# Kernel optimization log

Measured on AMD Instinct MI355X. Metric: run time of the kernel, lower is better.

## Reference

```python
import jax, jax.numpy as jnp
import numpy as np

W = 4           # cp_size (simulated ranks)
NUM_HEADS = 32
HEAD_SIZE = 128
NUM_KV_HEADS = 8
BLOCK_SIZE = 16
NUM_BLOCKS = 1024
MAX_BLOCKS = 32
MAX_CTX = 512   # <= _PARTITION_SIZE so single-partition stats are exact
NUM_SEQS = 32
SCALE = 1.0 / np.sqrt(HEAD_SIZE)
NEG_INF = -1e30


def setup_inputs() -> dict:
    key = jax.random.key(0)
    k1, k2, k3, k4, k5 = jax.random.split(key, 5)
    query = jax.random.normal(k1, (NUM_SEQS, 1, NUM_HEADS * HEAD_SIZE), dtype=jnp.float32)
    # per-rank paged KV caches, layout [W, num_blocks, kv_heads, block_size, head_size]
    key_cache = jax.random.normal(k2, (W, NUM_BLOCKS, NUM_KV_HEADS, BLOCK_SIZE, HEAD_SIZE), dtype=jnp.float32)
    value_cache = jax.random.normal(k3, (W, NUM_BLOCKS, NUM_KV_HEADS, BLOCK_SIZE, HEAD_SIZE), dtype=jnp.float32)
    block_tables = jax.random.randint(k4, (W, NUM_SEQS, MAX_BLOCKS), 0, NUM_BLOCKS, dtype=jnp.int32)
    context_lens = jax.random.randint(k5, (W, NUM_SEQS), 1, MAX_CTX + 1, dtype=jnp.int32)
    return {"query": query, "key_cache": key_cache, "value_cache": value_cache,
            "block_tables": block_tables, "context_lens": context_lens}


def reference(query, key_cache, value_cache, block_tables, context_lens):
    B, L, _ = query.shape
    S = B * L                       # num_seqs (decode: L=1)
    G = NUM_KV_HEADS
    Q = NUM_HEADS // G              # queries per kv head
    T = MAX_BLOCKS * BLOCK_SIZE     # max context per rank

    q = query.reshape(S, G, Q, HEAD_SIZE)
    ridx = jnp.arange(W)[:, None, None]
    # gather paged blocks: [W, S, MAX_BLOCKS, G, BLOCK_SIZE, D] -> [W, S, G, T, D]
    k = key_cache[ridx, block_tables].transpose(0, 1, 3, 2, 4, 5).reshape(W, S, G, T, HEAD_SIZE)
    v = value_cache[ridx, block_tables].transpose(0, 1, 3, 2, 4, 5).reshape(W, S, G, T, HEAD_SIZE)

    logits = jnp.einsum('sgqd,wsgtd->wsgqt', q, k) * SCALE
    mask = jnp.arange(T)[None, None, None, None, :] < context_lens[:, :, None, None, None]
    logits = jnp.where(mask, logits, NEG_INF)

    # per-rank online-softmax stats (== paged_attention_v2 single-partition output)
    m = jnp.max(logits, axis=-1)                      # [W,S,G,Q] max logit per rank
    p = jnp.exp(logits - m[..., None])
    p = jnp.where(mask, p, 0.0)
    esum = jnp.sum(p, axis=-1)                        # [W,S,G,Q]
    out_r = jnp.einsum('wsgqt,wsgtd->wsgqd', p, v) / esum[..., None]  # normalized per-rank out

    # cross-rank log-sum-exp reduction (distributed_paged_attention_v2_reduce)
    gmax = jnp.max(m, axis=0)                         # [S,G,Q]
    w_r = esum * jnp.exp(m - gmax[None])              # [W,S,G,Q]
    out = jnp.sum(out_r * w_r[..., None], axis=0) / jnp.sum(w_r, axis=0)[..., None]

    return out.reshape(B, L, NUM_HEADS * HEAD_SIZE)
```

## Files before the change

kernel.cpp:

```cpp
#include <hip/hip_runtime.h>
#include <math.h>

#define W 4
#define NUM_HEADS 32
#define HEAD_SIZE 128
#define G 8
#define QPG 4
#define BLOCK_SZ 16
#define NUM_BLOCKS 1024
#define MAX_BLOCKS 32
#define S 32
#define SPLIT 2
#define NPART (W * SPLIT)
#define SCALE 0.08838834764831845f
#define NEG_BIG (-1e30f)

#define BLK_STRIDE (G * BLOCK_SZ * HEAD_SIZE)
#define WG_STRIDE  (NUM_BLOCKS * BLK_STRIDE)

__global__ __launch_bounds__(256, 5)
void pa_partial_kernel(const float* __restrict__ query,
                       const float* __restrict__ key_cache,
                       const float* __restrict__ value_cache,
                       const int* __restrict__ block_tables,
                       const int* __restrict__ context_lens,
                       float* __restrict__ acc_ws,
                       float* __restrict__ m_ws,
                       float* __restrict__ e_ws)
{
    int bx = blockIdx.x;
    const int p = bx % SPLIT; bx /= SPLIT;
    const int g = bx % G;     bx /= G;
    const int s = bx % S;
    const int w = bx / S;

    const int tid   = threadIdx.x;
    const int accid = tid >> 5;
    const int lane  = tid & 31;
    const int d0    = lane * 4;
    const int h     = accid + 8 * p;

    __shared__ int   bt_lds[MAX_BLOCKS];
    __shared__ float sm_m[8][QPG];
    __shared__ float sm_e[8][QPG];
    __shared__ float sm_acc[8][QPG][HEAD_SIZE];

    if (tid < MAX_BLOCKS)
        bt_lds[tid] = block_tables[((size_t)w * S + s) * MAX_BLOCKS + tid];
    __syncthreads();

    float4 qf[QPG];
#pragma unroll
    for (int qi = 0; qi < QPG; ++qi)
        qf[qi] = *reinterpret_cast<const float4*>(
            query + ((size_t)s * NUM_HEADS + g * QPG + qi) * HEAD_SIZE + d0);

    const int ctx = context_lens[w * S + s];
    const float* kbase = key_cache   + (size_t)w * WG_STRIDE + (size_t)g * BLOCK_SZ * HEAD_SIZE;
    const float* vbase = value_cache + (size_t)w * WG_STRIDE + (size_t)g * BLOCK_SZ * HEAD_SIZE;

    float  m_i[QPG], e_i[QPG];
    float4 acc[QPG];
#pragma unroll
    for (int qi = 0; qi < QPG; ++qi) {
        m_i[qi] = NEG_BIG; e_i[qi] = 0.f;
        acc[qi] = make_float4(0.f, 0.f, 0.f, 0.f);
    }

    for (int t = h; t < ctx; t += 2 * 16) {
        const int off1 = bt_lds[t >> 4] * BLK_STRIDE + (t & 15) * HEAD_SIZE + d0;
        const float4 k1 = *reinterpret_cast<const float4*>(kbase + off1);
        const float4 v1 = *reinterpret_cast<const float4*>(vbase + off1);
        const int  t2   = t + 16;
        const bool vld2 = t2 < ctx;
        float4 k2 = make_float4(0.f, 0.f, 0.f, 0.f);
        float4 v2 = make_float4(0.f, 0.f, 0.f, 0.f);
        if (vld2) {
            const int off2 = bt_lds[t2 >> 4] * BLK_STRIDE + (t2 & 15) * HEAD_SIZE + d0;
            k2 = *reinterpret_cast<const float4*>(kbase + off2);
            v2 = *reinterpret_cast<const float4*>(vbase + off2);
        }

        float4 dv1, dv2;
        dv1.x = qf[0].x*k1.x + qf[0].y*k1.y + qf[0].z*k1.z + qf[0].w*k1.w;
        dv1.y = qf[1].x*k1.x + qf[1].y*k1.y + qf[1].z*k1.z + qf[1].w*k1.w;
        dv1.z = qf[2].x*k1.x + qf[2].y*k1.y + qf[2].z*k1.z + qf[2].w*k1.w;
        dv1.w = qf[3].x*k1.x + qf[3].y*k1.y + qf[3].z*k1.z + qf[3].w*k1.w;
        dv2.x = qf[0].x*k2.x + qf[0].y*k2.y + qf[0].z*k2.z + qf[0].w*k2.w;
        dv2.y = qf[1].x*k2.x + qf[1].y*k2.y + qf[1].z*k2.z + qf[1].w*k2.w;
        dv2.z = qf[2].x*k2.x + qf[2].y*k2.y + qf[2].z*k2.z + qf[2].w*k2.w;
        dv2.w = qf[3].x*k2.x + qf[3].y*k2.y + qf[3].z*k2.z + qf[3].w*k2.w;
#pragma unroll
        for (int o = 16; o > 0; o >>= 1) {
            dv1.x += __shfl_xor(dv1.x, o); dv1.y += __shfl_xor(dv1.y, o);
            dv1.z += __shfl_xor(dv1.z, o); dv1.w += __shfl_xor(dv1.w, o);
            dv2.x += __shfl_xor(dv2.x, o); dv2.y += __shfl_xor(dv2.y, o);
            dv2.z += __shfl_xor(dv2.z, o); dv2.w += __shfl_xor(dv2.w, o);
        }
        const float l1[QPG] = {dv1.x*SCALE, dv1.y*SCALE, dv1.z*SCALE, dv1.w*SCALE};
        float l2[QPG] = {dv2.x*SCALE, dv2.y*SCALE, dv2.z*SCALE, dv2.w*SCALE};
#pragma unroll
        for (int qi = 0; qi < QPG; ++qi) if (!vld2) l2[qi] = NEG_BIG;

#pragma unroll
        for (int qi = 0; qi < QPG; ++qi) {
            const float mn    = fmaxf(m_i[qi], fmaxf(l1[qi], l2[qi]));
            const float alpha = __expf(m_i[qi] - mn);
            const float p1    = __expf(l1[qi] - mn);
            const float p2    = __expf(l2[qi] - mn);
            m_i[qi] = mn;
            e_i[qi] = e_i[qi] * alpha + (p1 + p2);
            acc[qi].x = fmaf(acc[qi].x, alpha, fmaf(p1, v1.x, p2 * v2.x));
            acc[qi].y = fmaf(acc[qi].y, alpha, fmaf(p1, v1.y, p2 * v2.y));
            acc[qi].z = fmaf(acc[qi].z, alpha, fmaf(p1, v1.z, p2 * v2.z));
            acc[qi].w = fmaf(acc[qi].w, alpha, fmaf(p1, v1.w, p2 * v2.w));
        }
    }

#pragma unroll
    for (int qi = 0; qi < QPG; ++qi) {
        if (lane == 0) { sm_m[accid][qi] = m_i[qi]; sm_e[accid][qi] = e_i[qi]; }
        sm_acc[accid][qi][d0 + 0] = acc[qi].x;
        sm_acc[accid][qi][d0 + 1] = acc[qi].y;
        sm_acc[accid][qi][d0 + 2] = acc[qi].z;
        sm_acc[accid][qi][d0 + 3] = acc[qi].w;
    }
    __syncthreads();

    const int r = w * SPLIT + p;
    for (int pi = tid; pi < QPG * HEAD_SIZE; pi += 256) {
        const int qi = pi >> 7;
        const int d  = pi & (HEAD_SIZE - 1);
        float gm = NEG_BIG;
#pragma unroll
        for (int hh = 0; hh < 8; ++hh) gm = fmaxf(gm, sm_m[hh][qi]);
        float num = 0.f, den = 0.f;
#pragma unroll
        for (int hh = 0; hh < 8; ++hh) {
            const float sc = __expf(sm_m[hh][qi] - gm);
            num += sm_acc[hh][qi][d] * sc;
            den += sm_e[hh][qi] * sc;
        }
        const size_t idx = (((size_t)r * S + s) * G + g) * QPG + qi;
        acc_ws[idx * HEAD_SIZE + d] = num;
        if (d == 0) { m_ws[idx] = gm; e_ws[idx] = den; }
    }
}

__global__ __launch_bounds__(256)
void pa_reduce_kernel(const float* __restrict__ acc_ws,
                      const float* __restrict__ m_ws,
                      const float* __restrict__ e_ws,
                      float* __restrict__ out)
{
    const int bx = blockIdx.x;
    const int s = bx / G, g = bx % G;
    const int tid = threadIdx.x;
    for (int pi = tid; pi < QPG * HEAD_SIZE; pi += 256) {
        const int qi = pi >> 7;
        const int d  = pi & (HEAD_SIZE - 1);
        float mw[NPART], ew[NPART];
        float gm = NEG_BIG;
#pragma unroll
        for (int r = 0; r < NPART; ++r) {
            const size_t idx = (((size_t)r * S + s) * G + g) * QPG + qi;
            mw[r] = m_ws[idx];
            ew[r] = e_ws[idx];
            gm = fmaxf(gm, mw[r]);
        }
        float num = 0.f, den = 0.f;
#pragma unroll
        for (int r = 0; r < NPART; ++r) {
            const float sc = __expf(mw[r] - gm);
            const size_t idx = (((size_t)r * S + s) * G + g) * QPG + qi;
            num += acc_ws[idx * HEAD_SIZE + d] * sc;
            den += ew[r] * sc;
        }
        out[((size_t)s * NUM_HEADS + g * QPG + qi) * HEAD_SIZE + d] = num / den;
    }
}

__global__ __launch_bounds__(256)
void pa_fused_kernel(const float* __restrict__ query,
                     const float* __restrict__ key_cache,
                     const float* __restrict__ value_cache,
                     const int* __restrict__ block_tables,
                     const int* __restrict__ context_lens,
                     float* __restrict__ out)
{
    const int bx = blockIdx.x;
    const int s = bx / G, g = bx % G;
    const int tid   = threadIdx.x;
    const int accid = tid >> 5;
    const int lane  = tid & 31;
    const int d0    = lane * 4;

    __shared__ int   bt_lds[MAX_BLOCKS];
    __shared__ float sm_m[8][QPG];
    __shared__ float sm_e[8][QPG];
    __shared__ float sm_acc[8][QPG][HEAD_SIZE];

    float4 qf[QPG];
#pragma unroll
    for (int qi = 0; qi < QPG; ++qi)
        qf[qi] = *reinterpret_cast<const float4*>(
            query + ((size_t)s * NUM_HEADS + g * QPG + qi) * HEAD_SIZE + d0);

    float  m_i[QPG], e_i[QPG];
    float4 acc[QPG];
#pragma unroll
    for (int qi = 0; qi < QPG; ++qi) {
        m_i[qi] = NEG_BIG; e_i[qi] = 0.f;
        acc[qi] = make_float4(0.f, 0.f, 0.f, 0.f);
    }

    for (int w = 0; w < W; ++w) {
        __syncthreads();
        if (tid < MAX_BLOCKS)
            bt_lds[tid] = block_tables[((size_t)w * S + s) * MAX_BLOCKS + tid];
        __syncthreads();
        const int ctx = context_lens[w * S + s];
        const float* kbase = key_cache   + (size_t)w * WG_STRIDE + (size_t)g * BLOCK_SZ * HEAD_SIZE;
        const float* vbase = value_cache + (size_t)w * WG_STRIDE + (size_t)g * BLOCK_SZ * HEAD_SIZE;
        for (int t = accid; t < ctx; t += 8) {
            const int off = bt_lds[t >> 4] * BLK_STRIDE + (t & 15) * HEAD_SIZE + d0;
            const float4 kx = *reinterpret_cast<const float4*>(kbase + off);
            const float4 vx = *reinterpret_cast<const float4*>(vbase + off);
            float4 dv;
            dv.x = qf[0].x*kx.x + qf[0].y*kx.y + qf[0].z*kx.z + qf[0].w*kx.w;
            dv.y = qf[1].x*kx.x + qf[1].y*kx.y + qf[1].z*kx.z + qf[1].w*kx.w;
            dv.z = qf[2].x*kx.x + qf[2].y*kx.y + qf[2].z*kx.z + qf[2].w*kx.w;
            dv.w = qf[3].x*kx.x + qf[3].y*kx.y + qf[3].z*kx.z + qf[3].w*kx.w;
#pragma unroll
            for (int o = 16; o > 0; o >>= 1) {
                dv.x += __shfl_xor(dv.x, o); dv.y += __shfl_xor(dv.y, o);
                dv.z += __shfl_xor(dv.z, o); dv.w += __shfl_xor(dv.w, o);
            }
            const float lg[QPG] = {dv.x*SCALE, dv.y*SCALE, dv.z*SCALE, dv.w*SCALE};
#pragma unroll
            for (int qi = 0; qi < QPG; ++qi) {
                const float mn    = fmaxf(m_i[qi], lg[qi]);
                const float alpha = __expf(m_i[qi] - mn);
                const float pp    = __expf(lg[qi] - mn);
                m_i[qi] = mn;
                e_i[qi] = e_i[qi] * alpha + pp;
                acc[qi].x = fmaf(acc[qi].x, alpha, pp * vx.x);
                acc[qi].y = fmaf(acc[qi].y, alpha, pp * vx.y);
                acc[qi].z = fmaf(acc[qi].z, alpha, pp * vx.z);
                acc[qi].w = fmaf(acc[qi].w, alpha, pp * vx.w);
            }
        }
    }

#pragma unroll
    for (int qi = 0; qi < QPG; ++qi) {
        if (lane == 0) { sm_m[accid][qi] = m_i[qi]; sm_e[accid][qi] = e_i[qi]; }
        sm_acc[accid][qi][d0 + 0] = acc[qi].x;
        sm_acc[accid][qi][d0 + 1] = acc[qi].y;
        sm_acc[accid][qi][d0 + 2] = acc[qi].z;
        sm_acc[accid][qi][d0 + 3] = acc[qi].w;
    }
    __syncthreads();

    for (int pi = tid; pi < QPG * HEAD_SIZE; pi += 256) {
        const int qi = pi >> 7;
        const int d  = pi & (HEAD_SIZE - 1);
        float gm = NEG_BIG;
#pragma unroll
        for (int hh = 0; hh < 8; ++hh) gm = fmaxf(gm, sm_m[hh][qi]);
        float num = 0.f, den = 0.f;
#pragma unroll
        for (int hh = 0; hh < 8; ++hh) {
            const float sc = __expf(sm_m[hh][qi] - gm);
            num += sm_acc[hh][qi][d] * sc;
            den += sm_e[hh][qi] * sc;
        }
        out[((size_t)s * NUM_HEADS + g * QPG + qi) * HEAD_SIZE + d] = num / den;
    }
}

extern "C" void kernel_launch(void* const* d_in, const int* in_sizes, int n_in,
                              void* d_out, int out_size, void* d_ws, size_t ws_size,
                              hipStream_t stream) {
    const float* query        = (const float*)d_in[0];
    const float* key_cache    = (const float*)d_in[1];
    const float* value_cache  = (const float*)d_in[2];
    const int*   block_tables = (const int*)d_in[3];
    const int*   context_lens = (const int*)d_in[4];
    float* out = (float*)d_out;

    const size_t n_acc   = (size_t)NPART * S * G * QPG * HEAD_SIZE;
    const size_t n_stats = (size_t)NPART * S * G * QPG;
    const size_t need    = (n_acc + 2 * n_stats) * sizeof(float);

    if (ws_size >= need) {
        float* acc_ws = (float*)d_ws;
        float* m_ws   = acc_ws + n_acc;
        float* e_ws   = m_ws + n_stats;
        pa_partial_kernel<<<W * S * G * SPLIT, 256, 0, stream>>>(
            query, key_cache, value_cache, block_tables, context_lens,
            acc_ws, m_ws, e_ws);
        pa_reduce_kernel<<<S * G, 256, 0, stream>>>(acc_ws, m_ws, e_ws, out);
    } else {
        pa_fused_kernel<<<S * G, 256, 0, stream>>>(
            query, key_cache, value_cache, block_tables, context_lens, out);
    }
}
```

Before: 460.2 us.

## Use DPP lane reductions and lazy shared-max softmax rescaling in paged attention

Replaces the shuffle-based butterfly reduction of the QK dot products with DPP row operations plus one cross-row shuffle. The online softmax now keeps a single running max shared across the four query heads, padded by a margin so rescaling happens only when that max is exceeded, and computes exponentials as exp2 of a fused multiply-add. The main loop is split into a full two-token body and a single-token tail, which removes per-iteration validity masking. The shared max with a margin can lose precision for query heads whose logits sit well below the group max, and it makes the per-warp rescale branch divergent.

```diff
diff --git a/kernel.cpp b/kernel.cpp
--- a/kernel.cpp
+++ b/kernel.cpp
@@ -14,9 +14,27 @@
 #define NPART (W * SPLIT)
 #define SCALE 0.08838834764831845f
 #define NEG_BIG (-1e30f)
+#define L2E 1.4426950408889634f
+#define K1L2E (SCALE * L2E)
+#define RESCALE_MARGIN 4.0f
 
 #define BLK_STRIDE (G * BLOCK_SZ * HEAD_SIZE)
 #define WG_STRIDE  (NUM_BLOCKS * BLK_STRIDE)
+
+template <int CTRL>
+__device__ __forceinline__ float dpp_fold(float x) {
+    const int y = __builtin_amdgcn_update_dpp(0, __float_as_int(x), CTRL, 0xF, 0xF, true);
+    return x + __int_as_float(y);
+}
+
+__device__ __forceinline__ float half_allsum(float x) {
+    x = dpp_fold<0xB1>(x);
+    x = dpp_fold<0x4E>(x);
+    x = dpp_fold<0x141>(x);
+    x = dpp_fold<0x140>(x);
+    x += __shfl_xor(x, 16);
+    return x;
+}
 
 __global__ __launch_bounds__(256, 5)
 void pa_partial_kernel(const float* __restrict__ query,
@@ -41,7 +59,7 @@
     const int h     = accid + 8 * p;
 
     __shared__ int   bt_lds[MAX_BLOCKS];
-    __shared__ float sm_m[8][QPG];
+    __shared__ float sm_m[8];
     __shared__ float sm_e[8][QPG];
     __shared__ float sm_acc[8][QPG][HEAD_SIZE];
 
@@ -59,67 +77,103 @@
     const float* kbase = key_cache   + (size_t)w * WG_STRIDE + (size_t)g * BLOCK_SZ * HEAD_SIZE;
     const float* vbase = value_cache + (size_t)w * WG_STRIDE + (size_t)g * BLOCK_SZ * HEAD_SIZE;
 
-    float  m_i[QPG], e_i[QPG];
+    float m_run = NEG_BIG;
+    float bexp  = 0.f;
+    float e_i[QPG];
     float4 acc[QPG];
 #pragma unroll
     for (int qi = 0; qi < QPG; ++qi) {
-        m_i[qi] = NEG_BIG; e_i[qi] = 0.f;
+        e_i[qi] = 0.f;
         acc[qi] = make_float4(0.f, 0.f, 0.f, 0.f);
     }
 
-    for (int t = h; t < ctx; t += 2 * 16) {
+    int t = h;
+    for (; t + 16 < ctx; t += 32) {
+        const int slot = (t & 15) * HEAD_SIZE + d0;
+        const int off1 = bt_lds[t >> 4] * BLK_STRIDE + slot;
+        const int off2 = bt_lds[(t >> 4) + 1] * BLK_STRIDE + slot;
+        const float4 k1 = *reinterpret_cast<const float4*>(kbase + off1);
+        const float4 k2 = *reinterpret_cast<const float4*>(kbase + off2);
+        const float4 v1 = *reinterpret_cast<const float4*>(vbase + off1);
+        const float4 v2 = *reinterpret_cast<const float4*>(vbase + off2);
+
+        float dA[QPG], dB[QPG];
+#pragma unroll
+        for (int qi = 0; qi < QPG; ++qi) {
+            dA[qi] = qf[qi].x*k1.x + qf[qi].y*k1.y + qf[qi].z*k1.z + qf[qi].w*k1.w;
+            dB[qi] = qf[qi].x*k2.x + qf[qi].y*k2.y + qf[qi].z*k2.z + qf[qi].w*k2.w;
+        }
+#pragma unroll
+        for (int qi = 0; qi < QPG; ++qi) {
+            dA[qi] = half_allsum(dA[qi]);
+            dB[qi] = half_allsum(dB[qi]);
+        }
+
+        float mraw = fmaxf(fmaxf(dA[0], dA[1]), fmaxf(dA[2], dA[3]));
+        mraw = fmaxf(mraw, fmaxf(fmaxf(dB[0], dB[1]), fmaxf(dB[2], dB[3])));
+        const float mx = mraw * SCALE;
+        if (mx > m_run) {
+            const float newm  = mx + RESCALE_MARGIN;
+            const float alpha = exp2f((m_run - newm) * L2E);
+            m_run = newm;
+            bexp  = -m_run * L2E;
+#pragma unroll
+            for (int qi = 0; qi < QPG; ++qi) {
+                e_i[qi] *= alpha;
+                acc[qi].x *= alpha; acc[qi].y *= alpha;
+                acc[qi].z *= alpha; acc[qi].w *= alpha;
+            }
+        }
+#pragma unroll
+        for (int qi = 0; qi < QPG; ++qi) {
+            const float p1 = exp2f(fmaf(dA[qi], K1L2E, bexp));
+            const float p2 = exp2f(fmaf(dB[qi], K1L2E, bexp));
+            e_i[qi] += p1 + p2;
+            acc[qi].x = fmaf(p2, v2.x, fmaf(p1, v1.x, acc[qi].x));
+            acc[qi].y = fmaf(p2, v2.y, fmaf(p1, v1.y, acc[qi].y));
+            acc[qi].z = fmaf(p2, v2.z, fmaf(p1, v1.z, acc[qi].z));
+            acc[qi].w = fmaf(p2, v2.w, fmaf(p1, v1.w, acc[qi].w));
+        }
+    }
+    if (t < ctx) {
         const int off1 = bt_lds[t >> 4] * BLK_STRIDE + (t & 15) * HEAD_SIZE + d0;
         const float4 k1 = *reinterpret_cast<const float4*>(kbase + off1);
         const float4 v1 = *reinterpret_cast<const float4*>(vbase + off1);
-        const int  t2   = t + 16;
-        const bool vld2 = t2 < ctx;
-        float4 k2 = make_float4(0.f, 0.f, 0.f, 0.f);
-        float4 v2 = make_float4(0.f, 0.f, 0.f, 0.f);
-        if (vld2) {
-            const int off2 = bt_lds[t2 >> 4] * BLK_STRIDE + (t2 & 15) * HEAD_SIZE + d0;
-            k2 = *reinterpret_cast<const float4*>(kbase + off2);
-            v2 = *reinterpret_cast<const float4*>(vbase + off2);
-        }
-
-        float4 dv1, dv2;
-        dv1.x = qf[0].x*k1.x + qf[0].y*k1.y + qf[0].z*k1.z + qf[0].w*k1.w;
-        dv1.y = qf[1].x*k1.x + qf[1].y*k1.y + qf[1].z*k1.z + qf[1].w*k1.w;
-        dv1.z = qf[2].x*k1.x + qf[2].y*k1.y + qf[2].z*k1.z + qf[2].w*k1.w;
-        dv1.w = qf[3].x*k1.x + qf[3].y*k1.y + qf[3].z*k1.z + qf[3].w*k1.w;
-        dv2.x = qf[0].x*k2.x + qf[0].y*k2.y + qf[0].z*k2.z + qf[0].w*k2.w;
-        dv2.y = qf[1].x*k2.x + qf[1].y*k2.y + qf[1].z*k2.z + qf[1].w*k2.w;
-        dv2.z = qf[2].x*k2.x + qf[2].y*k2.y + qf[2].z*k2.z + qf[2].w*k2.w;
-        dv2.w = qf[3].x*k2.x + qf[3].y*k2.y + qf[3].z*k2.z + qf[3].w*k2.w;
-#pragma unroll
-        for (int o = 16; o > 0; o >>= 1) {
-            dv1.x += __shfl_xor(dv1.x, o); dv1.y += __shfl_xor(dv1.y, o);
-            dv1.z += __shfl_xor(dv1.z, o); dv1.w += __shfl_xor(dv1.w, o);
-            dv2.x += __shfl_xor(dv2.x, o); dv2.y += __shfl_xor(dv2.y, o);
-            dv2.z += __shfl_xor(dv2.z, o); dv2.w += __shfl_xor(dv2.w, o);
-        }
-        const float l1[QPG] = {dv1.x*SCALE, dv1.y*SCALE, dv1.z*SCALE, dv1.w*SCALE};
-        float l2[QPG] = {dv2.x*SCALE, dv2.y*SCALE, dv2.z*SCALE, dv2.w*SCALE};
-#pragma unroll
-        for (int qi = 0; qi < QPG; ++qi) if (!vld2) l2[qi] = NEG_BIG;
-
+        float dA[QPG];
+#pragma unroll
+        for (int qi = 0; qi < QPG; ++qi)
+            dA[qi] = qf[qi].x*k1.x + qf[qi].y*k1.y + qf[qi].z*k1.z + qf[qi].w*k1.w;
+#pragma unroll
+        for (int qi = 0; qi < QPG; ++qi)
+            dA[qi] = half_allsum(dA[qi]);
+        const float mx = SCALE * fmaxf(fmaxf(dA[0], dA[1]), fmaxf(dA[2], dA[3]));
+        if (mx > m_run) {
+            const float newm  = mx + RESCALE_MARGIN;
+            const float alpha = exp2f((m_run - newm) * L2E);
+            m_run = newm;
+            bexp  = -m_run * L2E;
+#pragma unroll
+            for (int qi = 0; qi < QPG; ++qi) {
+                e_i[qi] *= alpha;
+                acc[qi].x *= alpha; acc[qi].y *= alpha;
+                acc[qi].z *= alpha; acc[qi].w *= alpha;
+            }
+        }
 #pragma unroll
         for (int qi = 0; qi < QPG; ++qi) {
-            const float mn    = fmaxf(m_i[qi], fmaxf(l1[qi], l2[qi]));
-            const float alpha = __expf(m_i[qi] - mn);
-            const float p1    = __expf(l1[qi] - mn);
-            const float p2    = __expf(l2[qi] - mn);
-            m_i[qi] = mn;
-            e_i[qi] = e_i[qi] * alpha + (p1 + p2);
-            acc[qi].x = fmaf(acc[qi].x, alpha, fmaf(p1, v1.x, p2 * v2.x));
-            acc[qi].y = fmaf(acc[qi].y, alpha, fmaf(p1, v1.y, p2 * v2.y));
-            acc[qi].z = fmaf(acc[qi].z, alpha, fmaf(p1, v1.z, p2 * v2.z));
-            acc[qi].w = fmaf(acc[qi].w, alpha, fmaf(p1, v1.w, p2 * v2.w));
-        }
-    }
-
+            const float p1 = exp2f(fmaf(dA[qi], K1L2E, bexp));
+            e_i[qi] += p1;
+            acc[qi].x = fmaf(p1, v1.x, acc[qi].x);
+            acc[qi].y = fmaf(p1, v1.y, acc[qi].y);
+            acc[qi].z = fmaf(p1, v1.z, acc[qi].z);
+            acc[qi].w = fmaf(p1, v1.w, acc[qi].w);
+        }
+    }
+
+    if (lane == 0) sm_m[accid] = m_run;
 #pragma unroll
     for (int qi = 0; qi < QPG; ++qi) {
-        if (lane == 0) { sm_m[accid][qi] = m_i[qi]; sm_e[accid][qi] = e_i[qi]; }
+        if (lane == 0) sm_e[accid][qi] = e_i[qi];
         sm_acc[accid][qi][d0 + 0] = acc[qi].x;
         sm_acc[accid][qi][d0 + 1] = acc[qi].y;
         sm_acc[accid][qi][d0 + 2] = acc[qi].z;
@@ -128,18 +182,21 @@
     __syncthreads();
 
     const int r = w * SPLIT + p;
+    float gm = NEG_BIG;
+#pragma unroll
+    for (int hh = 0; hh < 8; ++hh) gm = fmaxf(gm, sm_m[hh]);
+    float sc[8];
+#pragma unroll
+    for (int hh = 0; hh < 8; ++hh) sc[hh] = __expf(sm_m[hh] - gm);
+
     for (int pi = tid; pi < QPG * HEAD_SIZE; pi += 256) {
         const int qi = pi >> 7;
         const int d  = pi & (HEAD_SIZE - 1);
-        float gm = NEG_BIG;
-#pragma unroll
-        for (int hh = 0; hh < 8; ++hh) gm = fmaxf(gm, sm_m[hh][qi]);
         float num = 0.f, den = 0.f;
 #pragma unroll
         for (int hh = 0; hh < 8; ++hh) {
-            const float sc = __expf(sm_m[hh][qi] - gm);
-            num += sm_acc[hh][qi][d] * sc;
-            den += sm_e[hh][qi] * sc;
+            num += sm_acc[hh][qi][d] * sc[hh];
+            den += sm_e[hh][qi] * sc[hh];
         }
         const size_t idx = (((size_t)r * S + s) * G + g) * QPG + qi;
         acc_ws[idx * HEAD_SIZE + d] = num;
@@ -226,22 +283,19 @@
             const int off = bt_lds[t >> 4] * BLK_STRIDE + (t & 15) * HEAD_SIZE + d0;
             const float4 kx = *reinterpret_cast<const float4*>(kbase + off);
             const float4 vx = *reinterpret_cast<const float4*>(vbase + off);
-            float4 dv;
-            dv.x = qf[0].x*kx.x + qf[0].y*kx.y + qf[0].z*kx.z + qf[0].w*kx.w;
-            dv.y = qf[1].x*kx.x + qf[1].y*kx.y + qf[1].z*kx.z + qf[1].w*kx.w;
-            dv.z = qf[2].x*kx.x + qf[2].y*kx.y + qf[2].z*kx.z + qf[2].w*kx.w;
-            dv.w = qf[3].x*kx.x + qf[3].y*kx.y + qf[3].z*kx.z + qf[3].w*kx.w;
-#pragma unroll
-            for (int o = 16; o > 0; o >>= 1) {
-                dv.x += __shfl_xor(dv.x, o); dv.y += __shfl_xor(dv.y, o);
-                dv.z += __shfl_xor(dv.z, o); dv.w += __shfl_xor(dv.w, o);
-            }
-            const float lg[QPG] = {dv.x*SCALE, dv.y*SCALE, dv.z*SCALE, dv.w*SCALE};
+            float dv[QPG];
+#pragma unroll
+            for (int qi = 0; qi < QPG; ++qi)
+                dv[qi] = qf[qi].x*kx.x + qf[qi].y*kx.y + qf[qi].z*kx.z + qf[qi].w*kx.w;
+#pragma unroll
+            for (int qi = 0; qi < QPG; ++qi)
+                dv[qi] = half_allsum(dv[qi]);
 #pragma unroll
             for (int qi = 0; qi < QPG; ++qi) {
-                const float mn    = fmaxf(m_i[qi], lg[qi]);
+                const float lg    = dv[qi] * SCALE;
+                const float mn    = fmaxf(m_i[qi], lg);
                 const float alpha = __expf(m_i[qi] - mn);
-                const float pp    = __expf(lg[qi] - mn);
+                const float pp    = __expf(lg - mn);
                 m_i[qi] = mn;
                 e_i[qi] = e_i[qi] * alpha + pp;
                 acc[qi].x = fmaf(acc[qi].x, alpha, pp * vx.x);
```

After: 459.4 us. About the same (-0.2%).
